# Optimization experiments

Hardware: AMD Instinct MI355X
Metric: run time of the kernel (lower is better)

## Reference

```python
import jax, jax.numpy as jnp
import numpy as np

N, IN_C, OUT_C = 8192, 256, 256


def setup_inputs() -> dict:
    key = jax.random.key(0)
    k1, k2, k3 = jax.random.split(key, 3)
    x = jax.random.normal(k1, (N, IN_C), dtype=jnp.float32)
    adj = jax.random.uniform(k2, (N, N), dtype=jnp.float32)
    # learned parameter: torch.rand(in_channels, out_channels)
    w = jax.random.uniform(k3, (IN_C, OUT_C), dtype=jnp.float32)
    return {"x": x, "adj": adj, "w": w}


def reference(x, adj, w):
    # A = adj + I
    A = adj + jnp.eye(adj.shape[0], dtype=adj.dtype)
    # D_hat = sqrt(inv(diag(rowsum(A)))) == diag(deg^{-1/2}) since D is diagonal
    deg = jnp.sum(A, axis=1)                      # [N]
    d_isqrt = jax.lax.rsqrt(deg)                  # [N]
    # A_hat = D_hat @ A @ D_hat  ==  row/col scaling by d^{-1/2}
    A_hat = A * d_isqrt[:, None] * d_isqrt[None, :]
    # ELU((A_hat @ x) @ w)
    h = jnp.matmul(A_hat, x)                      # [N, in_c]
    return jax.nn.elu(jnp.matmul(h, w))           # [N, out_c]
```

## Files before the change

kernel.cpp:

```cpp
#include <hip/hip_runtime.h>
#include <stdint.h>

#define N_NODES 8192
#define CH 256
#define MT 32
#define BK 64
#define KB_COUNT 128
#define ZROWS 16
#define ZBLOCKS (N_NODES / ZROWS)
#define DEGBLOCKS (N_NODES / 4)

typedef __bf16 bf16x8 __attribute__((ext_vector_type(8)));
typedef float f32x4 __attribute__((ext_vector_type(4)));
typedef unsigned short u16x4 __attribute__((ext_vector_type(4)));

__device__ __forceinline__ void async_copy16(const void* g, void* l) {
  __builtin_amdgcn_global_load_lds(
      (const __attribute__((address_space(1))) void*)(uintptr_t)g,
      (__attribute__((address_space(3))) void*)(uint32_t)(uintptr_t)l,
      16, 0, 0);
}

__device__ __forceinline__ unsigned short f32_to_bf16_rne(float f) {
  unsigned u = __float_as_uint(f);
  u += 0x7FFFu + ((u >> 16) & 1u);
  return (unsigned short)(u >> 16);
}

__device__ __forceinline__ u16x4 f32x4_to_bf16_rne(f32x4 v) {
  u16x4 r;
  r.x = f32_to_bf16_rne(v.x);
  r.y = f32_to_bf16_rne(v.y);
  r.z = f32_to_bf16_rne(v.z);
  r.w = f32_to_bf16_rne(v.w);
  return r;
}

__global__ void __launch_bounds__(256) k_pass1(const float* __restrict__ x,
                                               const float* __restrict__ w,
                                               const float* __restrict__ adj,
                                               float* __restrict__ z,
                                               float* __restrict__ dsq,
                                               unsigned short* __restrict__ adjb) {
  __shared__ float xs[ZROWS][CH];
  if (blockIdx.x < ZBLOCKS) {
    const int r0 = blockIdx.x * ZROWS;
    const int t = threadIdx.x;
#pragma unroll
    for (int r = 0; r < ZROWS; ++r) xs[r][t] = x[(size_t)(r0 + r) * CH + t];
    __syncthreads();
    float acc[ZROWS];
#pragma unroll
    for (int r = 0; r < ZROWS; ++r) acc[r] = 0.f;
    for (int k = 0; k < CH; k += 8) {
      float wv[8];
#pragma unroll
      for (int u = 0; u < 8; ++u) wv[u] = w[(size_t)(k + u) * CH + t];
#pragma unroll
      for (int r = 0; r < ZROWS; ++r) {
#pragma unroll
        for (int u = 0; u < 8; ++u) acc[r] += xs[r][k + u] * wv[u];
      }
    }
#pragma unroll
    for (int r = 0; r < ZROWS; ++r) z[(size_t)(r0 + r) * CH + t] = acc[r];
  } else {
    const int wave = threadIdx.x >> 6, lane = threadIdx.x & 63;
    const int row = (blockIdx.x - ZBLOCKS) * 4 + wave;
    const f32x4* ar = (const f32x4*)(adj + (size_t)row * N_NODES);
    u16x4* br = (u16x4*)(adjb + (size_t)row * N_NODES);
    float s0 = 0.f, s1 = 0.f, s2 = 0.f, s3 = 0.f;
#pragma unroll
    for (int i = 0; i < 8; ++i) {
      f32x4 a = ar[lane + 64 * (4 * i + 0)];
      f32x4 b = ar[lane + 64 * (4 * i + 1)];
      f32x4 c = ar[lane + 64 * (4 * i + 2)];
      f32x4 d = ar[lane + 64 * (4 * i + 3)];
      br[lane + 64 * (4 * i + 0)] = f32x4_to_bf16_rne(a);
      br[lane + 64 * (4 * i + 1)] = f32x4_to_bf16_rne(b);
      br[lane + 64 * (4 * i + 2)] = f32x4_to_bf16_rne(c);
      br[lane + 64 * (4 * i + 3)] = f32x4_to_bf16_rne(d);
      s0 += (a.x + a.y) + (a.z + a.w);
      s1 += (b.x + b.y) + (b.z + b.w);
      s2 += (c.x + c.y) + (c.z + c.w);
      s3 += (d.x + d.y) + (d.z + d.w);
    }
    float s = (s0 + s1) + (s2 + s3);
#pragma unroll
    for (int off = 32; off > 0; off >>= 1) s += __shfl_down(s, off, 64);
    if (lane == 0) dsq[row] = rsqrtf(s + 1.0f);
  }
}

__global__ void __launch_bounds__(256) k_y(const float* __restrict__ z,
                                           const float* __restrict__ dsq,
                                           unsigned short* __restrict__ yt) {
  const int r0 = blockIdx.x * 16;
  const int t = threadIdx.x;
  unsigned short vals[16];
#pragma unroll
  for (int r = 0; r < 16; ++r)
    vals[r] = f32_to_bf16_rne(dsq[r0 + r] * z[(size_t)(r0 + r) * CH + t]);
  *(u16x4*)&yt[(size_t)t * N_NODES + r0 + 0] = *(u16x4*)&vals[0];
  *(u16x4*)&yt[(size_t)t * N_NODES + r0 + 4] = *(u16x4*)&vals[4];
  *(u16x4*)&yt[(size_t)t * N_NODES + r0 + 8] = *(u16x4*)&vals[8];
  *(u16x4*)&yt[(size_t)t * N_NODES + r0 + 12] = *(u16x4*)&vals[12];
}

__global__ void __launch_bounds__(512, 1) k_gemm1(const unsigned short* __restrict__ adjb,
                                                  const unsigned short* __restrict__ yt,
                                                  const float* __restrict__ z,
                                                  const float* __restrict__ dsq,
                                                  float* __restrict__ out) {
  __shared__ __align__(16) unsigned short As[2][MT * BK];
  __shared__ __align__(16) unsigned short Bs[2][CH * BK];

  const int tid = threadIdx.x;
  const int wave = tid >> 6;
  const int lane = tid & 63;
  const int m0 = blockIdx.x * MT;
  const int lr = lane & 15;
  const int lq = lane >> 4;

  const bool hasA = wave < 4;
  const unsigned short* ag;
  int aoffu;
  {
    int i = hasA ? wave : 0;
    int p = 64 * i + lane;
    int r = p >> 3;
    int c8 = (lane & 7) ^ (r & 7);
    ag = adjb + (size_t)(m0 + r) * N_NODES + c8 * 8;
    aoffu = 1024 * i;
  }
  const unsigned short* bg[4];
  int boffu[4];
#pragma unroll
  for (int q = 0; q < 4; ++q) {
    int i = wave * 4 + q;
    int p = 64 * i + lane;
    int n = p >> 3;
    int c8 = (lane & 7) ^ (n & 7);
    bg[q] = yt + (size_t)n * N_NODES + c8 * 8;
    boffu[q] = 1024 * i;
  }

  f32x4 acc[2][2];
#pragma unroll
  for (int i = 0; i < 2; ++i)
#pragma unroll
    for (int j = 0; j < 2; ++j) acc[i][j] = (f32x4){0.f, 0.f, 0.f, 0.f};

  auto issue = [&](int b, int k0) {
    char* aL = (char*)&As[b][0];
    char* bL = (char*)&Bs[b][0];
    if (hasA) async_copy16(ag + k0, aL + aoffu);
#pragma unroll
    for (int q = 0; q < 4; ++q) async_copy16(bg[q] + k0, bL + boffu[q]);
  };

  issue(0, 0);

  for (int kb = 0; kb < KB_COUNT; ++kb) {
    const int b = kb & 1;
    __syncthreads();
    if (kb + 1 < KB_COUNT) issue(b ^ 1, (kb + 1) * BK);

    const char* aB = (const char*)&As[b][0];
    const char* bB = (const char*)&Bs[b][0];

#pragma unroll
    for (int k32 = 0; k32 < 2; ++k32) {
      bf16x8 afr[2];
#pragma unroll
      for (int mt = 0; mt < 2; ++mt) {
        int row = mt * 16 + lr;
        int c8 = k32 * 4 + lq;
        int p = row * 8 + (c8 ^ (row & 7));
        afr[mt] = *(const bf16x8*)(aB + p * 16);
      }
#pragma unroll
      for (int nt = 0; nt < 2; ++nt) {
        int n = wave * 32 + nt * 16 + lr;
        int c8 = k32 * 4 + lq;
        int p = n * 8 + (c8 ^ (n & 7));
        bf16x8 bfr = *(const bf16x8*)(bB + p * 16);
        acc[0][nt] = __builtin_amdgcn_mfma_f32_16x16x32_bf16(afr[0], bfr, acc[0][nt], 0, 0, 0);
        acc[1][nt] = __builtin_amdgcn_mfma_f32_16x16x32_bf16(afr[1], bfr, acc[1][nt], 0, 0, 0);
      }
    }
  }

#pragma unroll
  for (int mt = 0; mt < 2; ++mt) {
#pragma unroll
    for (int r = 0; r < 4; ++r) {
      int row = m0 + mt * 16 + lq * 4 + r;
      float di = dsq[row];
#pragma unroll
      for (int nt = 0; nt < 2; ++nt) {
        int col = wave * 32 + nt * 16 + lr;
        float v = acc[mt][nt][r];
        v = di * (v + di * z[(size_t)row * CH + col]);
        v = v > 0.f ? v : expm1f(v);
        out[(size_t)row * CH + col] = v;
      }
    }
  }
}

extern "C" void kernel_launch(void* const* d_in, const int* in_sizes, int n_in,
                              void* d_out, int out_size, void* d_ws, size_t ws_size,
                              hipStream_t stream) {
  const float* x = (const float*)d_in[0];
  const float* adj = (const float*)d_in[1];
  const float* w = (const float*)d_in[2];
  float* out = (float*)d_out;

  float* dsq = (float*)d_ws;
  unsigned short* yt = (unsigned short*)((char*)d_ws + 32768);
  float* z = (float*)((char*)d_ws + 4227072);
  unsigned short* adjb = (unsigned short*)((char*)d_ws + 12615680);

  k_pass1<<<ZBLOCKS + DEGBLOCKS, 256, 0, stream>>>(x, w, adj, z, dsq, adjb);
  k_y<<<N_NODES / 16, 256, 0, stream>>>(z, dsq, yt);
  k_gemm1<<<N_NODES / MT, 512, 0, stream>>>(adjb, yt, z, dsq, out);
}
```

Baseline: 500.8 us.

## Deepen k_gemm1 LDS pipeline to four stages with explicit vmcnt waits

Replaces the double-buffered main loop of the aggregation GEMM with a 4-stage ring that keeps three tiles of async global-to-LDS loads in flight. It uses hand-placed s_waitcnt vmcnt counts (per-wave, depending on whether the wave loads A) plus raw s_barrier in place of __syncthreads. A peeled tail handles the last two stages. MFMA sections are also wrapped in s_setprio to favour matrix issue. The goal is to hide global/L2 latency for the streamed adjacency and Y tiles. In exchange, LDS use grows to about 144KB, and correctness now depends on the hand-computed wait counts.

Result: faster. 480.6 us (-4.0%).

```diff
diff --git a/kernel.cpp b/kernel.cpp
--- a/kernel.cpp
+++ b/kernel.cpp
@@ -6,6 +6,7 @@
 #define MT 32
 #define BK 64
 #define KB_COUNT 128
+#define NSTAGE 4
 #define ZROWS 16
 #define ZBLOCKS (N_NODES / ZROWS)
 #define DEGBLOCKS (N_NODES / 4)
@@ -112,8 +113,8 @@
                                                   const float* __restrict__ z,
                                                   const float* __restrict__ dsq,
                                                   float* __restrict__ out) {
-  __shared__ __align__(16) unsigned short As[2][MT * BK];
-  __shared__ __align__(16) unsigned short Bs[2][CH * BK];
+  __shared__ __align__(16) unsigned short As[NSTAGE][MT * BK];
+  __shared__ __align__(16) unsigned short Bs[NSTAGE][CH * BK];
 
   const int tid = threadIdx.x;
   const int wave = tid >> 6;
@@ -159,16 +160,9 @@
     for (int q = 0; q < 4; ++q) async_copy16(bg[q] + k0, bL + boffu[q]);
   };
 
-  issue(0, 0);
-
-  for (int kb = 0; kb < KB_COUNT; ++kb) {
-    const int b = kb & 1;
-    __syncthreads();
-    if (kb + 1 < KB_COUNT) issue(b ^ 1, (kb + 1) * BK);
-
+  auto compute = [&](int b) {
     const char* aB = (const char*)&As[b][0];
     const char* bB = (const char*)&Bs[b][0];
-
 #pragma unroll
     for (int k32 = 0; k32 < 2; ++k32) {
       bf16x8 afr[2];
@@ -179,6 +173,7 @@
         int p = row * 8 + (c8 ^ (row & 7));
         afr[mt] = *(const bf16x8*)(aB + p * 16);
       }
+      __builtin_amdgcn_s_setprio(1);
 #pragma unroll
       for (int nt = 0; nt < 2; ++nt) {
         int n = wave * 32 + nt * 16 + lr;
@@ -188,8 +183,33 @@
         acc[0][nt] = __builtin_amdgcn_mfma_f32_16x16x32_bf16(afr[0], bfr, acc[0][nt], 0, 0, 0);
         acc[1][nt] = __builtin_amdgcn_mfma_f32_16x16x32_bf16(afr[1], bfr, acc[1][nt], 0, 0, 0);
       }
-    }
-  }
+      __builtin_amdgcn_s_setprio(0);
+    }
+  };
+
+  issue(0, 0);
+  issue(1, BK);
+  issue(2, 2 * BK);
+
+  for (int kb = 0; kb < KB_COUNT - 2; ++kb) {
+    if (hasA) asm volatile("s_waitcnt vmcnt(10)" ::: "memory");
+    else      asm volatile("s_waitcnt vmcnt(8)"  ::: "memory");
+    __builtin_amdgcn_s_barrier();
+    __builtin_amdgcn_sched_barrier(0);
+    if (kb + 3 < KB_COUNT) issue((kb + 3) & (NSTAGE - 1), (kb + 3) * BK);
+    compute(kb & (NSTAGE - 1));
+    __builtin_amdgcn_sched_barrier(0);
+  }
+  if (hasA) asm volatile("s_waitcnt vmcnt(5)" ::: "memory");
+  else      asm volatile("s_waitcnt vmcnt(4)" ::: "memory");
+  __builtin_amdgcn_s_barrier();
+  __builtin_amdgcn_sched_barrier(0);
+  compute((KB_COUNT - 2) & (NSTAGE - 1));
+  __builtin_amdgcn_sched_barrier(0);
+  asm volatile("s_waitcnt vmcnt(0)" ::: "memory");
+  __builtin_amdgcn_s_barrier();
+  __builtin_amdgcn_sched_barrier(0);
+  compute((KB_COUNT - 1) & (NSTAGE - 1));
 
 #pragma unroll
   for (int mt = 0; mt < 2; ++mt) {
```
